# Performance work log

Hardware: AMD Instinct MI355X
Metric: run time of the kernel (lower is better)

The kernel has to match this reference:

```python
import jax, jax.numpy as jnp
import numpy as np

# Problem dims: K subcarriers, B batch, M users, NT antennas, NRF RF chains
K = 8; B = 64; M = 8; NT = 64; NRF = 8; N_ITER = 10
SIGMA2 = 1.0
LN2 = float(np.log(2.0))
EPS = 1e-4  # the +0.0001 in the F-gradient denominators
W_F_COM = 1.0; W_F_RAD = 0.5; W_W_COM = 1.0; W_W_RAD = 0.5


def _herm(X):
    return jnp.conj(jnp.swapaxes(X, -1, -2))


def _proj_unit(F, eps=1e-12):
    # project_unit_modulus (no active_mask path is used by execute_PGA)
    mag = jnp.abs(F)
    safe = jnp.where(mag > eps, mag, jnp.ones_like(mag))
    return jnp.where(mag > eps, F / safe, jnp.zeros_like(F))


def _grad_F_com(H, F, W):
    # Vectorized over the m-loop using rank-1 structure Htilde = h h^H.
    V = W @ _herm(W)                                  # [K,B,NRF,NRF]
    FV = F @ V                                        # [K,B,NT,NRF]
    a1 = jnp.einsum('kbmn,kbnr->kbmr', jnp.conj(H), FV)   # h^H F V
    g = jnp.einsum('kbnr,kbmn->kbmr', jnp.conj(F), H)     # F^H h
    Wm = jnp.swapaxes(W, -1, -2)                      # [K,B,M,NRF]
    s = jnp.einsum('kbmr,kbmr->kbm', jnp.conj(g), Wm)     # g^H w_m
    tr1 = jnp.real(jnp.einsum('kbmr,kbrs,kbms->kbm', jnp.conj(g), V, g))
    tr2 = tr1 - jnp.abs(s) ** 2                       # with V_mk = V - w w^H
    a2 = a1 - s[..., None] * jnp.conj(Wm)             # h^H F V_mk
    d1 = LN2 * (tr1 + SIGMA2) + EPS
    d2 = LN2 * (tr2 + SIGMA2) + EPS
    c = a1 / d1[..., None] - a2 / d2[..., None]
    gsum = jnp.einsum('kbmn,kbmr->kbnr', H, c)        # sum over m of h (.)
    return jnp.mean(gsum, axis=0)                     # sum over K / K -> [B,NT,NRF]


def _grad_F_rad(F, W, R):
    WWH = W @ _herm(W)
    FW = F @ WWH                                      # F W W^H
    E = FW @ _herm(F) - R                             # [K,B,NT,NT]
    gK = 2.0 * (E @ FW)
    rn = jnp.sum(jnp.abs(R[:, 0]) ** 2, axis=(-1, -2))  # ||R[k,0]||_F^2, [K]
    gK = gK / rn[:, None, None, None]                 # normalize_tau == 1
    return jnp.mean(gK, axis=0)                       # [B,NT,NRF]


def _grad_W_com(H, F, W):
    # In the source W_m == W, so denom_1 == denom_2 and only column m of
    # grad_W_1 survives the mask subtraction for each m.
    g = jnp.einsum('kbnr,kbmn->kbmr', jnp.conj(F), H)     # F^H h_m, [K,B,M,NRF]
    u = jnp.einsum('kbmr,kbrj->kbmj', g, jnp.conj(W))     # (W^H g_m)_j, [K,B,M,M]
    tr = jnp.sum(jnp.abs(u) ** 2, axis=-1)                # tr(W W^H Hbar_mk)
    d = LN2 * (tr + SIGMA2)                               # no eps in source
    u_mm = jnp.diagonal(u, axis1=-2, axis2=-1)            # [K,B,M]
    Gm = g * (jnp.conj(u_mm) / d)[..., None]              # [K,B,M,NRF]
    return jnp.swapaxes(Gm, -1, -2) / K                   # [K,B,NRF,M]


def _grad_W_rad(F, W, R):
    FW = F @ W
    E = FW @ _herm(FW) - R
    gW = 2.0 * (_herm(F) @ E @ FW)
    rn = jnp.sum(jnp.abs(R[:, 0]) ** 2, axis=(-1, -2))
    return gW / rn[:, None, None, None] / K               # [K,B,NRF,M]


def _sum_rate(H, F, W):
    g = jnp.einsum('kbnr,kbmn->kbmr', jnp.conj(F), H)     # F^H h_m
    t = jnp.einsum('kbmr,kbrj->kbmj', jnp.conj(g), W)     # g^H W, [K,B,M,M]
    tr1 = jnp.sum(jnp.abs(t) ** 2, axis=-1)
    tdiag = jnp.diagonal(t, axis1=-2, axis2=-1)
    tr2 = tr1 - jnp.abs(tdiag) ** 2
    rate = jnp.sum(jnp.log2((tr1 + SIGMA2) / (tr2 + SIGMA2)), axis=-1)  # [K,B]
    return jnp.mean(rate, axis=0)                         # [B]


def _beam_err(F, W, R):
    FW = F @ W
    E = FW @ _herm(FW) - R
    num = jnp.sum(jnp.abs(E) ** 2, axis=(-1, -2))         # [K,B]
    den = jnp.sum(jnp.abs(R[:, 0]) ** 2, axis=(-1, -2))   # [K]
    return jnp.mean(num / den[:, None], axis=0)           # [B]


def _normalize(F, W, Pt):
    # scale W per (k,b) so ||F W||_F^2 == Pt
    FW = F @ W
    nrm = jnp.sqrt(jnp.sum(jnp.abs(FW) ** 2, axis=(-1, -2)))
    scale = jnp.sqrt(jnp.float32(Pt)) / (nrm + 1e-12)
    return F, W * scale[..., None, None]


def _forward(H_re, H_im, R_re, R_im, F_re, F_im, W_re, W_im, step_size, Pt, n_iter):
    H = jax.lax.complex(H_re, H_im)
    R = jax.lax.complex(R_re, R_im)
    F = _proj_unit(jax.lax.complex(F_re, F_im))
    W = jax.lax.complex(W_re, W_im)
    F, W = _normalize(F, W, Pt)
    rates = [_sum_rate(H, F, W)]
    taus = [_beam_err(F, W, R)]
    for ii in range(n_iter):
        gFc = _grad_F_com(H, F, W)
        gFr = _grad_F_rad(F, W, R)
        F = F + step_size[ii, 0] * (W_F_COM * gFc - W_F_RAD * gFr)  # broadcast over K
        F = _proj_unit(F)
        gWc = _grad_W_com(H, F, W)
        gWr = _grad_W_rad(F, W, R)
        st = step_size[ii, 1:][:, None, None, None]                 # per-k step, [K,1,1,1]
        W = W + st * (W_W_COM * gWc - W_W_RAD * gWr)
        F, W = _normalize(F, W, Pt)
        rates.append(_sum_rate(H, F, W))
        taus.append(_beam_err(F, W, R))
    rates = jnp.stack(rates, axis=0).T   # [B, n_iter+1]
    taus = jnp.stack(taus, axis=0).T     # [B, n_iter+1]
    return rates, taus, F, W


def setup_inputs() -> dict:
    key = jax.random.key(0)
    ks = jax.random.split(key, 9)
    H_re = jax.random.normal(ks[0], (K, B, M, NT), jnp.float32)
    H_im = jax.random.normal(ks[1], (K, B, M, NT), jnp.float32)
    # Hermitian PSD radar covariance target R = X X^H / NT
    Xr = jax.random.normal(ks[2], (K, B, NT, NT), jnp.float32)
    Xi = jax.random.normal(ks[3], (K, B, NT, NT), jnp.float32)
    Xc = jax.lax.complex(Xr, Xi)
    Rc = (Xc @ _herm(Xc)) / NT
    F_re = jax.random.normal(ks[4], (K, B, NT, NRF), jnp.float32)
    F_im = jax.random.normal(ks[5], (K, B, NT, NRF), jnp.float32)
    W_re = jax.random.normal(ks[6], (K, B, NRF, M), jnp.float32)
    W_im = jax.random.normal(ks[7], (K, B, NRF, M), jnp.float32)
    step_size = 0.01 * jax.random.uniform(ks[8], (N_ITER, K + 1), jnp.float32)
    return {
        'H_re': H_re, 'H_im': H_im,
        'R_re': jnp.real(Rc).astype(jnp.float32), 'R_im': jnp.imag(Rc).astype(jnp.float32),
        'F_re': F_re, 'F_im': F_im, 'W_re': W_re, 'W_im': W_im,
        'step_size': step_size, 'Pt': 10, 'n_iter_outer': N_ITER,
    }


def reference(H_re, H_im, R_re, R_im, F_re, F_im, W_re, W_im, step_size, Pt, n_iter_outer):
    return _forward(H_re, H_im, R_re, R_im, F_re, F_im, W_re, W_im, step_size, Pt, n_iter_outer)
```

## Files before the change

### kernel.cpp

```cpp
#include <hip/hip_runtime.h>


typedef float2 cplx;

#define LN2F 0.69314718055994530942f

__device__ __forceinline__ cplx mkc(float x, float y){ return make_float2(x, y); }

__device__ __forceinline__ void cfma (cplx& a, cplx b, cplx c){
  a.x = fmaf(b.x, c.x, a.x); a.x = fmaf(-b.y, c.y, a.x);
  a.y = fmaf(b.x, c.y, a.y); a.y = fmaf( b.y, c.x, a.y);
}
__device__ __forceinline__ void cfmac(cplx& a, cplx b, cplx c){
  a.x = fmaf(b.x, c.x, a.x); a.x = fmaf( b.y, c.y, a.x);
  a.y = fmaf(b.x, c.y, a.y); a.y = fmaf(-b.y, c.x, a.y);
}
__device__ __forceinline__ void cfmacj(cplx& a, cplx b, cplx c){
  a.x = fmaf(b.x, c.x, a.x); a.x = fmaf( b.y, c.y, a.x);
  a.y = fmaf(-b.x, c.y, a.y); a.y = fmaf( b.y, c.x, a.y);
}
__device__ __forceinline__ cplx cmuljc(cplx b, cplx c){
  return mkc(b.x*c.x + b.y*c.y, b.y*c.x - b.x*c.y);
}

__device__ __forceinline__ void storeP(float2* p, cplx v){
  union { cplx f; unsigned long long u; } cv; cv.f = v;
  __hip_atomic_store((unsigned long long*)p, cv.u, __ATOMIC_RELAXED, __HIP_MEMORY_SCOPE_AGENT);
}
__device__ __forceinline__ cplx loadP(const float2* p){
  union { cplx f; unsigned long long u; } cv;
  cv.u = __hip_atomic_load((const unsigned long long*)p, __ATOMIC_RELAXED, __HIP_MEMORY_SCOPE_AGENT);
  return cv.f;
}

__device__ __forceinline__ float blockSum(float v, float* sred, int tid){
  #pragma unroll
  for (int off = 32; off > 0; off >>= 1) v += __shfl_down(v, off, 64);
  __syncthreads();
  if ((tid & 63) == 0) sred[tid >> 6] = v;
  __syncthreads();
  return sred[0] + sred[1] + sred[2] + sred[3];
}

template<bool TR>
__device__ __forceinline__ void type2r(const cplx* __restrict__ IN, const cplx* __restrict__ SM,
                                       int tid, cplx& o0, cplx& o1){
  const int n = tid & 63, w = tid >> 6;
  const int q0 = 2*w, q1 = 2*w + 1;
  cplx a = mkc(0.f,0.f), b = mkc(0.f,0.f);
  #pragma unroll
  for (int s = 0; s < 8; ++s){
    cplx in = IN[s*66 + n];
    cplx m0 = TR ? SM[q0*9 + s] : SM[s*9 + q0];
    cplx m1 = TR ? SM[q1*9 + s] : SM[s*9 + q1];
    cfma(a, in, m0);
    cfma(b, in, m1);
  }
  o0 = a; o1 = b;
}

template<bool TR>
__device__ __forceinline__ void type2s(const cplx* IN, const cplx* SM, cplx* OUT, int tid){
  cplx o0, o1;
  type2r<TR>(IN, SM, tid, o0, o1);
  const int n = tid & 63, w = tid >> 6;
  OUT[(2*w)*66 + n]   = o0;
  OUT[(2*w+1)*66 + n] = o1;
}

__device__ __forceinline__ cplx type3part(const cplx* __restrict__ P1, const cplx* __restrict__ P2, int tid){
  const int p = (tid >> 3) & 7, q = tid & 7, c = tid >> 6;
  const int n0 = c * 16;
  cplx a = mkc(0.f,0.f);
  #pragma unroll
  for (int nn = 0; nn < 16; ++nn){
    cfmac(a, P1[p*66 + n0 + nn], P2[q*66 + n0 + nn]);
  }
  return a;
}

__device__ __forceinline__ void t3gather(cplx* d0, cplx* d1, cplx* d2, int nops,
                                         const cplx* scr, int tid){
  if (tid < nops*64){
    int op = tid >> 6, pq = tid & 63;
    cplx a = scr[(0*nops+op)*64 + pq];
    cplx b = scr[(1*nops+op)*64 + pq];
    cplx c = scr[(2*nops+op)*64 + pq];
    cplx d = scr[(3*nops+op)*64 + pq];
    cplx r = mkc(a.x+b.x+c.x+d.x, a.y+b.y+c.y+d.y);
    cplx* dst = (op == 0) ? d0 : (op == 1) ? d1 : d2;
    dst[(pq>>3)*9 + (pq&7)] = r;
  }
}

__device__ __forceinline__ void computeRF(const cplx* Rreg, const cplx* sF_, cplx* sRF_,
                                          cplx* scr, int tid){
  const int l = tid & 63, w = tid >> 6;
  const int half = l >> 5;
  const int j0 = w*16 + half*8;
  cplx acc[16];
  #pragma unroll
  for (int q = 0; q < 16; ++q) acc[q] = mkc(0.f,0.f);
  #pragma unroll
  for (int jj = 0; jj < 8; ++jj){
    const int j = j0 + jj;
    cplx Ra = Rreg[2*jj], Rb = Rreg[2*jj+1];
    #pragma unroll
    for (int r = 0; r < 8; ++r){
      cplx f = sF_[r*66 + j];
      cfma(acc[r],   Ra, f);
      cfma(acc[8+r], Rb, f);
    }
  }
  #pragma unroll
  for (int q = 0; q < 16; ++q){
    acc[q].x += __shfl_xor(acc[q].x, 32, 64);
    acc[q].y += __shfl_xor(acc[q].y, 32, 64);
  }
  const int row = (half == 0) ? (l & 31) : ((l & 31) + 32);
  const int off = half ? 8 : 0;
  __syncthreads();
  if (w < 2){
    #pragma unroll
    for (int r = 0; r < 8; ++r) scr[w*576 + row*9 + r] = acc[off + r];
  }
  __syncthreads();
  if (w >= 2){
    const int base = (w-2)*576 + row*9;
    #pragma unroll
    for (int r = 0; r < 8; ++r){
      cplx t = scr[base + r];
      t.x += acc[off + r].x; t.y += acc[off + r].y;
      scr[base + r] = t;
    }
  }
  __syncthreads();
  #pragma unroll
  for (int o0 = 0; o0 < 2; ++o0){
    const int o = tid + o0*256;
    const int r = o >> 6, n = o & 63;
    cplx a = scr[n*9 + r], b = scr[576 + n*9 + r];
    sRF_[r*66 + n] = mkc(a.x + b.x, a.y + b.y);
  }
}

__device__ __forceinline__ void groupBarrier(unsigned* cnt, unsigned target, int tid){
  __syncthreads();
  if (tid == 0){
    __hip_atomic_fetch_add(cnt, 1u, __ATOMIC_RELAXED, __HIP_MEMORY_SCOPE_AGENT);
    while (__hip_atomic_load(cnt, __ATOMIC_RELAXED, __HIP_MEMORY_SCOPE_AGENT) < target){
      __builtin_amdgcn_s_sleep(1);
    }
  }
  __syncthreads();
}

__global__ __launch_bounds__(256, 2)
void pga_fused_kernel(float* __restrict__ H_re, float* __restrict__ H_im,
                      const float* __restrict__ R_re, const float* __restrict__ R_im,
                      float* __restrict__ F_re, float* __restrict__ F_im,
                      const float* __restrict__ W_re, const float* __restrict__ W_im,
                      const float* __restrict__ step_g, const int* __restrict__ PtA,
                      float* __restrict__ out, unsigned* __restrict__ bcnt,
                      int cstride)
{
  const int bid = blockIdx.x;
  const int kk = bid >> 6;
  const int bb = bid & 63;
  const int tid = threadIdx.x;
  const int l = tid & 63, w = tid >> 6;
  const size_t kb = (size_t)(kk*64 + bb);

  __shared__ cplx sF [528];
  __shared__ cplx sT [528];
  __shared__ cplx sRF[528];
  __shared__ cplx sH [528];
  __shared__ cplx sml[13*72];
  __shared__ cplx scr[1152];
  __shared__ float sD1[8], sD2[8], sredm[8];
  __shared__ cplx sSm[8];

  cplx* sW  = sml + 0*72;
  cplx* sV  = sml + 1*72;
  cplx* sG  = sml + 2*72;
  cplx* sA1 = sml + 3*72;
  cplx* sX  = sml + 4*72;
  cplx* sC  = sml + 5*72;
  cplx* sU  = sml + 6*72;
  cplx* sGWC= sml + 7*72;
  cplx* sTM = sml + 8*72;
  cplx* sA2 = sml + 9*72;
  cplx* sB2 = sml + 10*72;
  cplx* sC1 = sml + 11*72;
  cplx* sG2 = sml + 12*72;

  float* out_rates = out;
  float* out_taus  = out + 704;
  float* out_F = out + 1408;
  float* out_W = out + 1408 + 262144;

  unsigned* cnt = bcnt + bb*cstride;

  const float* Hre = H_re + kb*512;
  const float* Him = H_im + kb*512;
  const float* Fre = F_re + kb*512;
  const float* Fim = F_im + kb*512;
  const float* Wre = W_re + kb*64;
  const float* Wim = W_im + kb*64;
  const float* Rre = R_re + kb*4096;
  const float* Rim = R_im + kb*4096;

  #pragma unroll
  for (int o0 = 0; o0 < 2; ++o0){
    int o = tid + o0*256;
    int m = o >> 6, n = o & 63;
    sH[m*66 + n] = mkc(Hre[m*64 + n], Him[m*64 + n]);
  }
  #pragma unroll
  for (int o0 = 0; o0 < 2; ++o0){
    int o = tid + o0*256;
    int n = o >> 3, r = o & 7;
    float fr = Fre[n*8 + r], fi = Fim[n*8 + r];
    float mag = sqrtf(fr*fr + fi*fi);
    cplx v = (mag > 1e-12f) ? mkc(fr/mag, fi/mag) : mkc(0.f,0.f);
    sF[r*66 + n] = v;
  }
  if (tid < 64) sW[(tid>>3)*9 + (tid&7)] = mkc(Wre[tid], Wim[tid]);

  cplx Rreg[16];
  float rnp = 0.f;
  {
    const int rA = l & 31, rB = rA + 32;
    const int j0 = w*16 + (l >> 5)*8;
    const float4* a0 = (const float4*)(Rre + rA*64 + j0);
    const float4* a1 = (const float4*)(Rim + rA*64 + j0);
    const float4* b0 = (const float4*)(Rre + rB*64 + j0);
    const float4* b1 = (const float4*)(Rim + rB*64 + j0);
    float4 xr0 = a0[0], xr1 = a0[1], xi0 = a1[0], xi1 = a1[1];
    float4 yr0 = b0[0], yr1 = b0[1], yi0 = b1[0], yi1 = b1[1];
    Rreg[0]  = mkc(xr0.x, xi0.x); Rreg[2]  = mkc(xr0.y, xi0.y);
    Rreg[4]  = mkc(xr0.z, xi0.z); Rreg[6]  = mkc(xr0.w, xi0.w);
    Rreg[8]  = mkc(xr1.x, xi1.x); Rreg[10] = mkc(xr1.y, xi1.y);
    Rreg[12] = mkc(xr1.z, xi1.z); Rreg[14] = mkc(xr1.w, xi1.w);
    Rreg[1]  = mkc(yr0.x, yi0.x); Rreg[3]  = mkc(yr0.y, yi0.y);
    Rreg[5]  = mkc(yr0.z, yi0.z); Rreg[7]  = mkc(yr0.w, yi0.w);
    Rreg[9]  = mkc(yr1.x, yi1.x); Rreg[11] = mkc(yr1.y, yi1.y);
    Rreg[13] = mkc(yr1.z, yi1.z); Rreg[15] = mkc(yr1.w, yi1.w);
    #pragma unroll
    for (int q = 0; q < 16; ++q){
      rnp = fmaf(Rreg[q].x, Rreg[q].x, rnp);
      rnp = fmaf(Rreg[q].y, Rreg[q].y, rnp);
    }
  }
  float dp = 0.f;
  {
    const float* R0re = R_re + (size_t)(kk*64)*4096;
    const float* R0im = R_im + (size_t)(kk*64)*4096;
    for (int idx = tid; idx < 4096; idx += 256){
      float a = R0re[idx], c = R0im[idx];
      dp = fmaf(a, a, dp); dp = fmaf(c, c, dp);
    }
  }
  const float sqPt = sqrtf((float)PtA[0]);
  __syncthreads();

  const float Rnorm  = blockSum(rnp, sredm, tid);
  const float den    = blockSum(dp,  sredm, tid);
  const float invden = 1.f / den;

  {
    cplx w0, w1;
    type2r<false>(sF, sW, tid, w0, w1);
    float nn = w0.x*w0.x + w0.y*w0.y + w1.x*w1.x + w1.y*w1.y;
    float nrm2 = blockSum(nn, sredm, tid);
    float scale = sqPt / (sqrtf(nrm2) + 1e-12f);
    int n = tid & 63, w2 = tid >> 6;
    sT[(2*w2)*66 + n]   = mkc(w0.x*scale, w0.y*scale);
    sT[(2*w2+1)*66 + n] = mkc(w1.x*scale, w1.y*scale);
    if (tid < 64){
      cplx wv = sW[(tid>>3)*9 + (tid&7)];
      sW[(tid>>3)*9 + (tid&7)] = mkc(wv.x*scale, wv.y*scale);
    }
  }
  __syncthreads();

  { cplx pg = type3part(sF, sH, tid); scr[(tid>>6)*64 + (tid&63)] = pg; }
  __syncthreads();
  t3gather(sG, nullptr, nullptr, 1, scr, tid);
  __syncthreads();
  if (tid < 64){
    int m = tid >> 3, j = tid & 7;
    cplx a = mkc(0.f,0.f);
    #pragma unroll
    for (int r = 0; r < 8; ++r) cfmac(a, sG[r*9+m], sW[r*9+j]);
    sTM[m*9+j] = a;
  }
  __syncthreads();
  if (tid < 8){
    int m = tid; float t1 = 0.f;
    #pragma unroll
    for (int j = 0; j < 8; ++j){ cplx t = sTM[m*9+j]; t1 = fmaf(t.x,t.x,fmaf(t.y,t.y,t1)); }
    cplx td = sTM[m*9+m];
    float t2 = t1 - (td.x*td.x + td.y*td.y);
    sD2[m] = log2f((t1 + 1.f)/(t2 + 1.f));
  }
  __syncthreads();
  if (tid == 0){
    float rs = sD2[0]+sD2[1]+sD2[2]+sD2[3]+sD2[4]+sD2[5]+sD2[6]+sD2[7];
    atomicAdd(out_rates + bb*11 + 0, rs*0.125f);
  }
  computeRF(Rreg, sF, sRF, scr, tid);
  __syncthreads();
  { cplx pk = type3part(sT, sT, tid); scr[(tid>>6)*64 + (tid&63)] = pk; }
  __syncthreads();
  t3gather(sG2, nullptr, nullptr, 1, scr, tid);
  __syncthreads();
  {
    cplx r0, r1;
    type2r<false>(sRF, sW, tid, r0, r1);
    int n = tid & 63, w2 = tid >> 6;
    cplx a = sT[(2*w2)*66 + n], b = sT[(2*w2+1)*66 + n];
    float dotp = a.x*r0.x + a.y*r0.y + b.x*r1.x + b.y*r1.y;
    float Tt  = blockSum(dotp, sredm, tid);
    float g2v = 0.f;
    if (tid < 64){ cplx g = sG2[(tid>>3)*9 + (tid&7)]; g2v = g.x*g.x + g.y*g.y; }
    float G2s = blockSum(g2v, sredm, tid);
    if (tid == 0){
      float num = G2s - 2.f*Tt + Rnorm;
      atomicAdd(out_taus + bb*11 + 0, num*invden*0.125f);
    }
  }

  #pragma unroll 1
  for (int i = 0; i < 10; ++i){
    __syncthreads();
    if (tid < 64){
      int p = tid >> 3, q = tid & 7;
      cplx a = mkc(0.f,0.f);
      #pragma unroll
      for (int m = 0; m < 8; ++m) cfmac(a, sW[p*9+m], sW[q*9+m]);
      sV[p*9+q] = a;
    }
    __syncthreads();
    type2s<true>(sF, sV, sT, tid);
    __syncthreads();
    {
      cplx pa = type3part(sH, sT, tid);
      cplx pg = type3part(sF, sH, tid);
      int c = tid >> 6, pq = tid & 63;
      scr[(c*2+0)*64 + pq] = pa;
      scr[(c*2+1)*64 + pq] = pg;
    }
    __syncthreads();
    t3gather(sA1, sG, nullptr, 2, scr, tid);
    __syncthreads();
    if (tid < 8){
      cplx a = mkc(0.f,0.f);
      #pragma unroll
      for (int r = 0; r < 8; ++r) cfmac(a, sG[r*9+tid], sW[r*9+tid]);
      sSm[tid] = a;
    }
    if (tid < 64){
      int m = tid >> 3, r = tid & 7;
      cplx a = mkc(0.f,0.f);
      #pragma unroll
      for (int s2 = 0; s2 < 8; ++s2) cfma(a, sV[s2*9+r], sG[s2*9+m]);
      sTM[m*9+r] = a;
    }
    __syncthreads();
    if (tid < 8){
      int m = tid; float t1 = 0.f;
      #pragma unroll
      for (int r = 0; r < 8; ++r){
        cplx g = sG[r*9+m], vg = sTM[m*9+r];
        t1 = fmaf(g.x, vg.x, t1); t1 = fmaf(g.y, vg.y, t1);
      }
      cplx sm = sSm[m];
      float t2 = t1 - (sm.x*sm.x + sm.y*sm.y);
      sD1[m] = LN2F*(t1 + 1.f) + 1e-4f;
      sD2[m] = LN2F*(t2 + 1.f) + 1e-4f;
    }
    __syncthreads();
    if (tid < 64){
      int m = tid >> 3, r = tid & 7;
      cplx a1v = sA1[m*9+r];
      cplx sw = cmuljc(sSm[m], sW[r*9+m]);
      cplx a2v = mkc(a1v.x - sw.x, a1v.y - sw.y);
      float i1 = 1.f/sD1[m], i2 = 1.f/sD2[m];
      sC[m*9+r] = mkc(a1v.x*i1 - a2v.x*i2, a1v.y*i1 - a2v.y*i2);
    }
    __syncthreads();
    cplx f0, f1;
    type2r<false>(sH, sC, tid, f0, f1);

    { cplx px = type3part(sF, sT, tid); scr[(tid>>6)*64 + (tid&63)] = px; }
    __syncthreads();
    t3gather(sX, nullptr, nullptr, 1, scr, tid);
    __syncthreads();
    cplx x0, x1, v0, v1;
    type2r<false>(sT, sX, tid, x0, x1);
    type2r<true >(sRF, sV, tid, v0, v1);
    {
      int n = tid & 63, w2 = tid >> 6;
      float2* lo = (float2*)((i & 1) ? H_re : F_re) + kb*256;
      float2* hi = (float2*)((i & 1) ? H_im : F_im) + kb*256;
      cplx P0 = mkc((f0.x - (x0.x - v0.x)*invden)*0.125f,
                    (f0.y - (x0.y - v0.y)*invden)*0.125f);
      cplx P1 = mkc((f1.x - (x1.x - v1.x)*invden)*0.125f,
                    (f1.y - (x1.y - v1.y)*invden)*0.125f);
      int e0 = (2*w2)*64 + n;
      if (e0 < 256){ storeP(lo + e0, P0); storeP(lo + e0 + 64, P1); }
      else         { storeP(hi + e0 - 256, P0); storeP(hi + e0 - 192, P1); }
    }
    groupBarrier(cnt, 8u*(i+1), tid);

    {
      const float step0 = step_g[i*9];
      const float2* baseLo = (const float2*)((i & 1) ? H_re : F_re);
      const float2* baseHi = (const float2*)((i & 1) ? H_im : F_im);
      #pragma unroll
      for (int o0 = 0; o0 < 2; ++o0){
        int o = tid + o0*256;
        int r = o >> 6, n = o & 63;
        const float2* base = (o < 256) ? baseLo : baseHi;
        int eloc = o & 255;
        cplx acc = mkc(0.f,0.f);
        #pragma unroll
        for (int kp = 0; kp < 8; ++kp){
          cplx pv = loadP(base + (size_t)(kp*64 + bb)*256 + eloc);
          acc.x += pv.x; acc.y += pv.y;
        }
        cplx Fv = sF[r*66 + n];
        Fv.x = fmaf(step0, acc.x, Fv.x);
        Fv.y = fmaf(step0, acc.y, Fv.y);
        float mag = sqrtf(Fv.x*Fv.x + Fv.y*Fv.y);
        if (mag > 1e-12f){ Fv.x /= mag; Fv.y /= mag; } else { Fv = mkc(0.f,0.f); }
        sF[r*66 + n] = Fv;
      }
    }
    __syncthreads();
    computeRF(Rreg, sF, sRF, scr, tid);
    __syncthreads();
    { cplx pg = type3part(sF, sH, tid); scr[(tid>>6)*64 + (tid&63)] = pg; }
    __syncthreads();
    t3gather(sG, nullptr, nullptr, 1, scr, tid);
    __syncthreads();
    if (tid < 64){
      int m = tid >> 3, j = tid & 7;
      cplx a = mkc(0.f,0.f);
      #pragma unroll
      for (int r = 0; r < 8; ++r) cfmacj(a, sG[r*9+m], sW[r*9+j]);
      sU[m*9+j] = a;
    }
    __syncthreads();
    if (tid < 8){
      int m = tid; float tr = 0.f;
      #pragma unroll
      for (int j = 0; j < 8; ++j){ cplx u = sU[m*9+j]; tr = fmaf(u.x,u.x,fmaf(u.y,u.y,tr)); }
      sD1[m] = LN2F*(tr + 1.f);
    }
    __syncthreads();
    if (tid < 64){
      int r = tid >> 3, m = tid & 7;
      cplx t = cmuljc(sG[r*9+m], sU[m*9+m]);
      float f = 0.125f / sD1[m];
      sGWC[r*9+m] = mkc(t.x*f, t.y*f);
    }
    __syncthreads();
    type2s<false>(sF, sW, sT, tid);
    __syncthreads();
    {
      cplx pa = type3part(sF, sT, tid);
      cplx pb = type3part(sT, sT, tid);
      cplx pc = type3part(sF, sRF, tid);
      int c = tid >> 6, pq = tid & 63;
      scr[(c*3+0)*64 + pq] = pa;
      scr[(c*3+1)*64 + pq] = pb;
      scr[(c*3+2)*64 + pq] = pc;
    }
    __syncthreads();
    t3gather(sA2, sB2, sC1, 3, scr, tid);
    __syncthreads();
    {
      cplx ab = mkc(0.f,0.f), cw = mkc(0.f,0.f);
      int r = tid >> 3, m = tid & 7;
      if (tid < 64){
        #pragma unroll
        for (int m2 = 0; m2 < 8; ++m2) cfma(ab, sA2[r*9+m2], sB2[m2*9+m]);
        #pragma unroll
        for (int s2 = 0; s2 < 8; ++s2) cfma(cw, sC1[r*9+s2], sW[s2*9+m]);
      }
      __syncthreads();
      if (tid < 64){
        float st = step_g[i*9 + 1 + kk];
        cplx gwc = sGWC[r*9+m];
        float fac = invden*0.125f;
        float dx = gwc.x - (ab.x - cw.x)*fac;
        float dy = gwc.y - (ab.y - cw.y)*fac;
        cplx wv = sW[r*9+m];
        wv.x = fmaf(st, dx, wv.x);
        wv.y = fmaf(st, dy, wv.y);
        sW[r*9+m] = wv;
      }
    }
    __syncthreads();
    {
      cplx w0, w1;
      type2r<false>(sF, sW, tid, w0, w1);
      float nn = w0.x*w0.x + w0.y*w0.y + w1.x*w1.x + w1.y*w1.y;
      float nrm2 = blockSum(nn, sredm, tid);
      float scale = sqPt / (sqrtf(nrm2) + 1e-12f);
      int n = tid & 63, w2 = tid >> 6;
      sT[(2*w2)*66 + n]   = mkc(w0.x*scale, w0.y*scale);
      sT[(2*w2+1)*66 + n] = mkc(w1.x*scale, w1.y*scale);
      if (tid < 64){
        cplx wv = sW[(tid>>3)*9 + (tid&7)];
        sW[(tid>>3)*9 + (tid&7)] = mkc(wv.x*scale, wv.y*scale);
      }
    }
    __syncthreads();
    if (tid < 64){
      int m = tid >> 3, j = tid & 7;
      cplx a = mkc(0.f,0.f);
      #pragma unroll
      for (int r = 0; r < 8; ++r) cfmac(a, sG[r*9+m], sW[r*9+j]);
      sTM[m*9+j] = a;
    }
    __syncthreads();
    if (tid < 8){
      int m = tid; float t1 = 0.f;
      #pragma unroll
      for (int j = 0; j < 8; ++j){ cplx t = sTM[m*9+j]; t1 = fmaf(t.x,t.x,fmaf(t.y,t.y,t1)); }
      cplx td = sTM[m*9+m];
      float t2 = t1 - (td.x*td.x + td.y*td.y);
      sD2[m] = log2f((t1 + 1.f)/(t2 + 1.f));
    }
    __syncthreads();
    if (tid == 0){
      float rs = sD2[0]+sD2[1]+sD2[2]+sD2[3]+sD2[4]+sD2[5]+sD2[6]+sD2[7];
      atomicAdd(out_rates + bb*11 + (i+1), rs*0.125f);
    }
    { cplx pk = type3part(sT, sT, tid); scr[(tid>>6)*64 + (tid&63)] = pk; }
    __syncthreads();
    t3gather(sG2, nullptr, nullptr, 1, scr, tid);
    __syncthreads();
    {
      cplx r0, r1;
      type2r<false>(sRF, sW, tid, r0, r1);
      int n = tid & 63, w2 = tid >> 6;
      cplx a = sT[(2*w2)*66 + n], b = sT[(2*w2+1)*66 + n];
      float dotp = a.x*r0.x + a.y*r0.y + b.x*r1.x + b.y*r1.y;
      float Tt  = blockSum(dotp, sredm, tid);
      float g2v = 0.f;
      if (tid < 64){ cplx g = sG2[(tid>>3)*9 + (tid&7)]; g2v = g.x*g.x + g.y*g.y; }
      float G2s = blockSum(g2v, sredm, tid);
      if (tid == 0){
        float num = G2s - 2.f*Tt + Rnorm;
        atomicAdd(out_taus + bb*11 + (i+1), num*invden*0.125f);
      }
    }
  }

  __syncthreads();
  #pragma unroll
  for (int o0 = 0; o0 < 2; ++o0){
    int o = tid + o0*256;
    int n = o >> 3, r = o & 7;
    out_F[kb*512 + o] = sF[r*66 + n].x;
  }
  if (tid < 64){
    out_W[kb*64 + tid] = sW[(tid>>3)*9 + (tid&7)].x;
  }
}

extern "C" void kernel_launch(void* const* d_in, const int* in_sizes, int n_in,
                              void* d_out, int out_size, void* d_ws, size_t ws_size,
                              hipStream_t stream) {
  float* H_re = (float*)d_in[0];
  float* H_im = (float*)d_in[1];
  const float* R_re = (const float*)d_in[2];
  const float* R_im = (const float*)d_in[3];
  float* F_re = (float*)d_in[4];
  float* F_im = (float*)d_in[5];
  const float* W_re = (const float*)d_in[6];
  const float* W_im = (const float*)d_in[7];
  const float* step = (const float*)d_in[8];
  const int*   PtA  = (const int*)d_in[9];
  float* out = (float*)d_out;

  unsigned* bcnt = (unsigned*)d_ws;
  int cstride = (ws_size >= 4096) ? 16 : 1;
  size_t cbytes = (size_t)64 * 4 * (size_t)cstride;
  if (cbytes > ws_size) cbytes = ws_size;

  hipMemsetAsync(d_ws, 0, cbytes, stream);
  hipMemsetAsync(d_out, 0, 1408*sizeof(float), stream);

  pga_fused_kernel<<<dim3(512), dim3(256), 0, stream>>>(
      H_re, H_im, R_re, R_im, F_re, F_im, W_re, W_im,
      step, PtA, out, bcnt, cstride);
}
```

Before: 341.0 us.

## Cut block barriers by merging reductions and fusing per-iteration phases

Merges paired block reductions into a single two-value reduction, and folds the sF·sT type3 gather into the first gather of each iteration. The W-gradient denominator computation is fused into the step update, and the rate/tau atomics are combined at the end of the iteration. computeRF now writes all four wave partials to a larger scratch buffer and sums them in one pass, removing a barrier stage. The aim is fewer __syncthreads per PGA iteration, at the cost of more shared memory (a doubled scratch array), which may reduce occupancy.

```diff
diff --git a/kernel.cpp b/kernel.cpp
--- a/kernel.cpp
+++ b/kernel.cpp
@@ -4,6 +4,7 @@
 typedef float2 cplx;
 
 #define LN2F 0.69314718055994530942f
+#define GOFF 2048
 
 __device__ __forceinline__ cplx mkc(float x, float y){ return make_float2(x, y); }
 
@@ -40,6 +41,20 @@
   if ((tid & 63) == 0) sred[tid >> 6] = v;
   __syncthreads();
   return sred[0] + sred[1] + sred[2] + sred[3];
+}
+
+__device__ __forceinline__ void blockSum2(float v1, float v2, float* sred, int tid,
+                                          float& o1, float& o2){
+  #pragma unroll
+  for (int off = 32; off > 0; off >>= 1){
+    v1 += __shfl_down(v1, off, 64);
+    v2 += __shfl_down(v2, off, 64);
+  }
+  __syncthreads();
+  if ((tid & 63) == 0){ sred[tid >> 6] = v1; sred[4 + (tid >> 6)] = v2; }
+  __syncthreads();
+  o1 = sred[0] + sred[1] + sred[2] + sred[3];
+  o2 = sred[4] + sred[5] + sred[6] + sred[7];
 }
 
 template<bool TR>
@@ -120,27 +135,16 @@
   const int row = (half == 0) ? (l & 31) : ((l & 31) + 32);
   const int off = half ? 8 : 0;
   __syncthreads();
-  if (w < 2){
-    #pragma unroll
-    for (int r = 0; r < 8; ++r) scr[w*576 + row*9 + r] = acc[off + r];
-  }
-  __syncthreads();
-  if (w >= 2){
-    const int base = (w-2)*576 + row*9;
-    #pragma unroll
-    for (int r = 0; r < 8; ++r){
-      cplx t = scr[base + r];
-      t.x += acc[off + r].x; t.y += acc[off + r].y;
-      scr[base + r] = t;
-    }
-  }
+  #pragma unroll
+  for (int r = 0; r < 8; ++r) scr[w*576 + row*9 + r] = acc[off + r];
   __syncthreads();
   #pragma unroll
   for (int o0 = 0; o0 < 2; ++o0){
     const int o = tid + o0*256;
     const int r = o >> 6, n = o & 63;
-    cplx a = scr[n*9 + r], b = scr[576 + n*9 + r];
-    sRF_[r*66 + n] = mkc(a.x + b.x, a.y + b.y);
+    cplx a = scr[n*9 + r],        b = scr[576  + n*9 + r];
+    cplx c = scr[1152 + n*9 + r], d = scr[1728 + n*9 + r];
+    sRF_[r*66 + n] = mkc(a.x+b.x+c.x+d.x, a.y+b.y+c.y+d.y);
   }
 }
 
@@ -176,8 +180,8 @@
   __shared__ cplx sRF[528];
   __shared__ cplx sH [528];
   __shared__ cplx sml[13*72];
-  __shared__ cplx scr[1152];
-  __shared__ float sD1[8], sD2[8], sredm[8];
+  __shared__ cplx scr[2304];
+  __shared__ float sD2[8], sredm[8];
   __shared__ cplx sSm[8];
 
   cplx* sW  = sml + 0*72;
@@ -187,7 +191,6 @@
   cplx* sX  = sml + 4*72;
   cplx* sC  = sml + 5*72;
   cplx* sU  = sml + 6*72;
-  cplx* sGWC= sml + 7*72;
   cplx* sTM = sml + 8*72;
   cplx* sA2 = sml + 9*72;
   cplx* sB2 = sml + 10*72;
@@ -264,8 +267,8 @@
   const float sqPt = sqrtf((float)PtA[0]);
   __syncthreads();
 
-  const float Rnorm  = blockSum(rnp, sredm, tid);
-  const float den    = blockSum(dp,  sredm, tid);
+  float Rnorm, den;
+  blockSum2(rnp, dp, sredm, tid, Rnorm, den);
   const float invden = 1.f / den;
 
   {
@@ -321,10 +324,10 @@
     int n = tid & 63, w2 = tid >> 6;
     cplx a = sT[(2*w2)*66 + n], b = sT[(2*w2+1)*66 + n];
     float dotp = a.x*r0.x + a.y*r0.y + b.x*r1.x + b.y*r1.y;
-    float Tt  = blockSum(dotp, sredm, tid);
     float g2v = 0.f;
     if (tid < 64){ cplx g = sG2[(tid>>3)*9 + (tid&7)]; g2v = g.x*g.x + g.y*g.y; }
-    float G2s = blockSum(g2v, sredm, tid);
+    float Tt, G2s;
+    blockSum2(dotp, g2v, sredm, tid, Tt, G2s);
     if (tid == 0){
       float num = G2s - 2.f*Tt + Rnorm;
       atomicAdd(out_taus + bb*11 + 0, num*invden*0.125f);
@@ -333,7 +336,6 @@
 
   #pragma unroll 1
   for (int i = 0; i < 10; ++i){
-    __syncthreads();
     if (tid < 64){
       int p = tid >> 3, q = tid & 7;
       cplx a = mkc(0.f,0.f);
@@ -347,13 +349,18 @@
     {
       cplx pa = type3part(sH, sT, tid);
       cplx pg = type3part(sF, sH, tid);
+      cplx px = type3part(sF, sT, tid);
       int c = tid >> 6, pq = tid & 63;
-      scr[(c*2+0)*64 + pq] = pa;
-      scr[(c*2+1)*64 + pq] = pg;
-    }
-    __syncthreads();
-    t3gather(sA1, sG, nullptr, 2, scr, tid);
-    __syncthreads();
+      scr[(c*3+0)*64 + pq] = pa;
+      scr[(c*3+1)*64 + pq] = pg;
+      scr[(c*3+2)*64 + pq] = px;
+    }
+    __syncthreads();
+    t3gather(sA1, sG, sX, 3, scr, tid);
+    __syncthreads();
+    cplx x0, x1, v0, v1;
+    type2r<false>(sT, sX, tid, x0, x1);
+    type2r<true >(sRF, sV, tid, v0, v1);
     if (tid < 8){
       cplx a = mkc(0.f,0.f);
       #pragma unroll
@@ -368,39 +375,28 @@
       sTM[m*9+r] = a;
     }
     __syncthreads();
-    if (tid < 8){
-      int m = tid; float t1 = 0.f;
-      #pragma unroll
-      for (int r = 0; r < 8; ++r){
-        cplx g = sG[r*9+m], vg = sTM[m*9+r];
+    if (tid < 64){
+      int m = tid >> 3, r = tid & 7;
+      float t1 = 0.f;
+      #pragma unroll
+      for (int rr = 0; rr < 8; ++rr){
+        cplx g = sG[rr*9+m], vg = sTM[m*9+rr];
         t1 = fmaf(g.x, vg.x, t1); t1 = fmaf(g.y, vg.y, t1);
       }
       cplx sm = sSm[m];
       float t2 = t1 - (sm.x*sm.x + sm.y*sm.y);
-      sD1[m] = LN2F*(t1 + 1.f) + 1e-4f;
-      sD2[m] = LN2F*(t2 + 1.f) + 1e-4f;
-    }
-    __syncthreads();
-    if (tid < 64){
-      int m = tid >> 3, r = tid & 7;
+      float d1 = LN2F*(t1 + 1.f) + 1e-4f;
+      float d2 = LN2F*(t2 + 1.f) + 1e-4f;
       cplx a1v = sA1[m*9+r];
-      cplx sw = cmuljc(sSm[m], sW[r*9+m]);
+      cplx sw = cmuljc(sm, sW[r*9+m]);
       cplx a2v = mkc(a1v.x - sw.x, a1v.y - sw.y);
-      float i1 = 1.f/sD1[m], i2 = 1.f/sD2[m];
+      float i1 = 1.f/d1, i2 = 1.f/d2;
       sC[m*9+r] = mkc(a1v.x*i1 - a2v.x*i2, a1v.y*i1 - a2v.y*i2);
     }
     __syncthreads();
-    cplx f0, f1;
-    type2r<false>(sH, sC, tid, f0, f1);
-
-    { cplx px = type3part(sF, sT, tid); scr[(tid>>6)*64 + (tid&63)] = px; }
-    __syncthreads();
-    t3gather(sX, nullptr, nullptr, 1, scr, tid);
-    __syncthreads();
-    cplx x0, x1, v0, v1;
-    type2r<false>(sT, sX, tid, x0, x1);
-    type2r<true >(sRF, sV, tid, v0, v1);
-    {
+    {
+      cplx f0, f1;
+      type2r<false>(sH, sC, tid, f0, f1);
       int n = tid & 63, w2 = tid >> 6;
       float2* lo = (float2*)((i & 1) ? H_re : F_re) + kb*256;
       float2* hi = (float2*)((i & 1) ? H_im : F_im) + kb*256;
@@ -441,34 +437,10 @@
     __syncthreads();
     computeRF(Rreg, sF, sRF, scr, tid);
     __syncthreads();
-    { cplx pg = type3part(sF, sH, tid); scr[(tid>>6)*64 + (tid&63)] = pg; }
-    __syncthreads();
-    t3gather(sG, nullptr, nullptr, 1, scr, tid);
-    __syncthreads();
-    if (tid < 64){
-      int m = tid >> 3, j = tid & 7;
-      cplx a = mkc(0.f,0.f);
-      #pragma unroll
-      for (int r = 0; r < 8; ++r) cfmacj(a, sG[r*9+m], sW[r*9+j]);
-      sU[m*9+j] = a;
-    }
-    __syncthreads();
-    if (tid < 8){
-      int m = tid; float tr = 0.f;
-      #pragma unroll
-      for (int j = 0; j < 8; ++j){ cplx u = sU[m*9+j]; tr = fmaf(u.x,u.x,fmaf(u.y,u.y,tr)); }
-      sD1[m] = LN2F*(tr + 1.f);
-    }
-    __syncthreads();
-    if (tid < 64){
-      int r = tid >> 3, m = tid & 7;
-      cplx t = cmuljc(sG[r*9+m], sU[m*9+m]);
-      float f = 0.125f / sD1[m];
-      sGWC[r*9+m] = mkc(t.x*f, t.y*f);
-    }
-    __syncthreads();
+    { cplx pg = type3part(sF, sH, tid); scr[GOFF + (tid>>6)*64 + (tid&63)] = pg; }
     type2s<false>(sF, sW, sT, tid);
     __syncthreads();
+    t3gather(sG, nullptr, nullptr, 1, scr + GOFF, tid);
     {
       cplx pa = type3part(sF, sT, tid);
       cplx pb = type3part(sT, sT, tid);
@@ -480,28 +452,40 @@
     }
     __syncthreads();
     t3gather(sA2, sB2, sC1, 3, scr, tid);
-    __syncthreads();
-    {
-      cplx ab = mkc(0.f,0.f), cw = mkc(0.f,0.f);
+    if (tid < 64){
+      int m = tid >> 3, j = tid & 7;
+      cplx a = mkc(0.f,0.f);
+      #pragma unroll
+      for (int r = 0; r < 8; ++r) cfmacj(a, sG[r*9+m], sW[r*9+j]);
+      sU[m*9+j] = a;
+    }
+    __syncthreads();
+    cplx ab = mkc(0.f,0.f), cw = mkc(0.f,0.f);
+    float dws = 1.f;
+    if (tid < 64){
       int r = tid >> 3, m = tid & 7;
-      if (tid < 64){
-        #pragma unroll
-        for (int m2 = 0; m2 < 8; ++m2) cfma(ab, sA2[r*9+m2], sB2[m2*9+m]);
-        #pragma unroll
-        for (int s2 = 0; s2 < 8; ++s2) cfma(cw, sC1[r*9+s2], sW[s2*9+m]);
-      }
-      __syncthreads();
-      if (tid < 64){
-        float st = step_g[i*9 + 1 + kk];
-        cplx gwc = sGWC[r*9+m];
-        float fac = invden*0.125f;
-        float dx = gwc.x - (ab.x - cw.x)*fac;
-        float dy = gwc.y - (ab.y - cw.y)*fac;
-        cplx wv = sW[r*9+m];
-        wv.x = fmaf(st, dx, wv.x);
-        wv.y = fmaf(st, dy, wv.y);
-        sW[r*9+m] = wv;
-      }
+      #pragma unroll
+      for (int m2 = 0; m2 < 8; ++m2) cfma(ab, sA2[r*9+m2], sB2[m2*9+m]);
+      #pragma unroll
+      for (int s2 = 0; s2 < 8; ++s2) cfma(cw, sC1[r*9+s2], sW[s2*9+m]);
+      float tr = 0.f;
+      #pragma unroll
+      for (int j = 0; j < 8; ++j){ cplx u = sU[m*9+j]; tr = fmaf(u.x,u.x,fmaf(u.y,u.y,tr)); }
+      dws = LN2F*(tr + 1.f);
+    }
+    __syncthreads();
+    if (tid < 64){
+      int r = tid >> 3, m = tid & 7;
+      cplx t = cmuljc(sG[r*9+m], sU[m*9+m]);
+      float f = 0.125f / dws;
+      float st = step_g[i*9 + 1 + kk];
+      float fac = invden*0.125f;
+      float dx = t.x*f - (ab.x - cw.x)*fac;
+      float dy = t.y*f - (ab.y - cw.y)*fac;
+      cplx wv = sW[r*9+m];
+      wv.x = fmaf(st, dx, wv.x);
+      wv.y = fmaf(st, dy, wv.y);
+      sW[r*9+m] = wv;
     }
     __syncthreads();
     {
@@ -526,7 +510,11 @@
       for (int r = 0; r < 8; ++r) cfmac(a, sG[r*9+m], sW[r*9+j]);
       sTM[m*9+j] = a;
     }
-    __syncthreads();
+    { cplx pk = type3part(sT, sT, tid); scr[(tid>>6)*64 + (tid&63)] = pk; }
+    __syncthreads();
+    cplx r0, r1;
+    type2r<false>(sRF, sW, tid, r0, r1);
+    t3gather(sG2, nullptr, nullptr, 1, scr, tid);
     if (tid < 8){
       int m = tid; float t1 = 0.f;
       #pragma unroll
@@ -535,33 +523,28 @@
       float t2 = t1 - (td.x*td.x + td.y*td.y);
       sD2[m] = log2f((t1 + 1.f)/(t2 + 1.f));
     }
-    __syncthreads();
-    if (tid == 0){
-      float rs = sD2[0]+sD2[1]+sD2[2]+sD2[3]+sD2[4]+sD2[5]+sD2[6]+sD2[7];
-      atomicAdd(out_rates + bb*11 + (i+1), rs*0.125f);
-    }
-    { cplx pk = type3part(sT, sT, tid); scr[(tid>>6)*64 + (tid&63)] = pk; }
-    __syncthreads();
-    t3gather(sG2, nullptr, nullptr, 1, scr, tid);
-    __syncthreads();
-    {
-      cplx r0, r1;
-      type2r<false>(sRF, sW, tid, r0, r1);
+    float dotp;
+    {
       int n = tid & 63, w2 = tid >> 6;
       cplx a = sT[(2*w2)*66 + n], b = sT[(2*w2+1)*66 + n];
-      float dotp = a.x*r0.x + a.y*r0.y + b.x*r1.x + b.y*r1.y;
-      float Tt  = blockSum(dotp, sredm, tid);
+      dotp = a.x*r0.x + a.y*r0.y + b.x*r1.x + b.y*r1.y;
+    }
+    __syncthreads();
+    {
       float g2v = 0.f;
       if (tid < 64){ cplx g = sG2[(tid>>3)*9 + (tid&7)]; g2v = g.x*g.x + g.y*g.y; }
-      float G2s = blockSum(g2v, sredm, tid);
+      float Tt, G2s;
+      blockSum2(dotp, g2v, sredm, tid, Tt, G2s);
       if (tid == 0){
+        float rs = sD2[0]+sD2[1]+sD2[2]+sD2[3]+sD2[4]+sD2[5]+sD2[6]+sD2[7];
+        atomicAdd(out_rates + bb*11 + (i+1), rs*0.125f);
         float num = G2s - 2.f*Tt + Rnorm;
         atomicAdd(out_taus + bb*11 + (i+1), num*invden*0.125f);
       }
     }
-  }
-
-  __syncthreads();
+    __syncthreads();
+  }
+
   #pragma unroll
   for (int o0 = 0; o0 < 2; ++o0){
     int o = tid + o0*256;
```

Measured after the change: 396.9 us. 1.16x slower.
